# Optimization experiments

Hardware: AMD Instinct MI355X
Metric: run time of the kernel (lower is better)

Reference implementation:

```python
import jax, jax.numpy as jnp
import numpy as np

B, S, F, D, H, L, FF, M, NH, D2, O = 4, 1024, 20, 512, 8, 4, 2048, 32, 3, 256, 1
HD = D // H


def ln(x, g, b, eps=1e-5):
    m = jnp.mean(x, -1, keepdims=True)
    v = jnp.mean((x - m) ** 2, -1, keepdims=True)
    return (x - m) / jnp.sqrt(v + eps) * g + b


def posenc(seq_len, d_model):
    pos = jnp.arange(seq_len, dtype=jnp.float32)[:, None]
    div = jnp.exp(jnp.arange(0, d_model, 2, dtype=jnp.float32) * (-np.log(10000.0) / d_model))
    pe = jnp.zeros((seq_len, d_model), jnp.float32)
    pe = pe.at[:, 0::2].set(jnp.sin(pos * div)).at[:, 1::2].set(jnp.cos(pos * div))
    return pe


def setup_inputs():
    key = jax.random.key(0)
    ks = iter(jax.random.split(key, 64))
    g = lambda shape, s=0.02: jax.random.normal(next(ks), shape, jnp.float32) * s
    z = lambda shape: jnp.zeros(shape, jnp.float32)
    o = lambda shape: jnp.ones(shape, jnp.float32)
    return {
        'x': jax.random.normal(next(ks), (B, S, F), jnp.float32),
        'in_W': g((F, D)), 'in_b': z((D,)), 'in_ln_g': o((D,)), 'in_ln_b': z((D,)),
        'ln1_g': o((L, D)), 'ln1_b': z((L, D)),
        'Wq': g((L, D, D)), 'bq': z((L, D)), 'Wk': g((L, D, D)), 'bk': z((L, D)),
        'Wv': g((L, D, D)), 'bv': z((L, D)), 'Wo': g((L, D, D)), 'bo': z((L, D)),
        'rel': g((L, 2 * M + 1, HD)),
        'ln2_g': o((L, D)), 'ln2_b': z((L, D)),
        'W1': g((L, D, FF)), 'b1': z((L, FF)), 'W2': g((L, FF, D)), 'b2': z((L, D)),
        'gWq': g((D, D)), 'gbq': z((D,)), 'gWk': g((D, D)), 'gbk': z((D,)),
        'gWv': g((D, D)), 'gbv': z((D,)), 'gWo': g((D, D)), 'gbo': z((D,)),
        'hW1': g((NH, D, D2)), 'hb1': z((NH, D2)), 'hln_g': o((NH, D2)), 'hln_b': z((NH, D2)),
        'hW2': g((NH, D2, O)), 'hb2': z((NH, O)),
    }


def _heads(xx, Wq, bq, Wk, bk, Wv, bv):
    # project and split into heads -> [B,H,S,HD]
    q = (xx @ Wq + bq).reshape(B, S, H, HD).transpose(0, 2, 1, 3)
    k = (xx @ Wk + bk).reshape(B, S, H, HD).transpose(0, 2, 1, 3)
    v = (xx @ Wv + bv).reshape(B, S, H, HD).transpose(0, 2, 1, 3)
    return q, k, v


def _block(x, l1g, l1b, Wq, bq, Wk, bk, Wv, bv, Wo, bo, rel, l2g, l2b, W1, b1, W2, b2):
    xn = ln(x, l1g, l1b)
    q, k, v = _heads(xn, Wq, bq, Wk, bk, Wv, bv)
    scores = jnp.einsum('bhqd,bhkd->bhqk', q, k) / jnp.sqrt(jnp.float32(HD))
    pos = jnp.arange(S)
    rel_idx = jnp.clip(pos[None, :] - pos[:, None], -M, M) + M  # [S,S]
    rel_enc = rel[rel_idx]  # [S,S,HD]
    # relative-position bias (NOT scaled by sqrt(HD), matching the torch code)
    scores = scores + jnp.einsum('bhqd,qkd->bhqk', q, rel_enc)
    w = jax.nn.softmax(scores, axis=-1)
    out = jnp.einsum('bhqk,bhkd->bhqd', w, v).transpose(0, 2, 1, 3).reshape(B, S, D)
    x = x + out @ Wo + bo
    xn = ln(x, l2g, l2b)
    ff = jax.nn.gelu(xn @ W1 + b1, approximate=False) @ W2 + b2
    return x + ff


def _forward(x, in_W, in_b, in_ln_g, in_ln_b, ln1_g, ln1_b, Wq, bq, Wk, bk, Wv, bv, Wo, bo, rel,
             ln2_g, ln2_b, W1, b1, W2, b2, gWq, gbq, gWk, gbk, gWv, gbv, gWo, gbo,
             hW1, hb1, hln_g, hln_b, hW2, hb2):
    h = ln(x @ in_W + in_b, in_ln_g, in_ln_b)
    h = h + posenc(S, D)[None]
    for l in range(L):
        h = _block(h, ln1_g[l], ln1_b[l], Wq[l], bq[l], Wk[l], bk[l], Wv[l], bv[l],
                   Wo[l], bo[l], rel[l], ln2_g[l], ln2_b[l], W1[l], b1[l], W2[l], b2[l])
    # global multi-head self-attention (standard scaled dot-product)
    q, k, v = _heads(h, gWq, gbq, gWk, gbk, gWv, gbv)
    w = jax.nn.softmax(jnp.einsum('bhqd,bhkd->bhqk', q, k) / jnp.sqrt(jnp.float32(HD)), axis=-1)
    go = jnp.einsum('bhqk,bhkd->bhqd', w, v).transpose(0, 2, 1, 3).reshape(B, S, D) @ gWo + gbo
    ctx = go[:, -1, :]  # last-timestep context [B,D]
    y = jnp.einsum('bd,hde->bhe', ctx, hW1) + hb1  # [B,NH,D2]
    y = jax.nn.relu(ln(y, hln_g, hln_b))
    return jnp.einsum('bhe,heo->bho', y, hW2) + hb2  # [B,NH,O]


def reference(x, in_W, in_b, in_ln_g, in_ln_b, ln1_g, ln1_b, Wq, bq, Wk, bk, Wv, bv, Wo, bo, rel,
              ln2_g, ln2_b, W1, b1, W2, b2, gWq, gbq, gWk, gbk, gWv, gbv, gWo, gbo,
              hW1, hb1, hln_g, hln_b, hW2, hb2):
    return _forward(x, in_W, in_b, in_ln_g, in_ln_b, ln1_g, ln1_b, Wq, bq, Wk, bk, Wv, bv, Wo, bo,
                    rel, ln2_g, ln2_b, W1, b1, W2, b2, gWq, gbq, gWk, gbk, gWv, gbv, gWo, gbo,
                    hW1, hb1, hln_g, hln_b, hW2, hb2)
```

## Files before the change

kernel.cpp:

```cpp
#include <hip/hip_runtime.h>
#include <math.h>

#define DEV __device__ __forceinline__

constexpr int BSD = 4 * 1024 * 512;

typedef __attribute__((ext_vector_type(8))) short bf16x8;
typedef __attribute__((ext_vector_type(4))) float f32x4;

typedef __attribute__((address_space(1))) const void global_cvoid;
typedef __attribute__((address_space(3))) void lds_void;

DEV ushort f2b(float f) {
  union { float f; uint u; } x{f};
  uint r = x.u + 0x7fff + ((x.u >> 16) & 1);
  return (ushort)(r >> 16);
}
DEV float b2f(ushort u) {
  union { uint u; float f; } x{(uint)u << 16};
  return x.f;
}
DEV int swz128(int b) { return b ^ (((b >> 7) & 7) << 4); }

DEV float wave_sum(float v) {
#pragma unroll
  for (int m = 32; m >= 1; m >>= 1) v += __shfl_xor(v, m, 64);
  return v;
}
DEV float wave_max(float v) {
#pragma unroll
  for (int m = 32; m >= 1; m >>= 1) v = fmaxf(v, __shfl_xor(v, m, 64));
  return v;
}
DEV float block_sum(float v, float* sm) {
  v = wave_sum(v);
  __syncthreads();
  if ((threadIdx.x & 63) == 0) sm[threadIdx.x >> 6] = v;
  __syncthreads();
  return sm[0] + sm[1] + sm[2] + sm[3];
}
DEV float block_max(float v, float* sm) {
  v = wave_max(v);
  __syncthreads();
  if ((threadIdx.x & 63) == 0) sm[threadIdx.x >> 6] = v;
  __syncthreads();
  return fmaxf(fmaxf(sm[0], sm[1]), fmaxf(sm[2], sm[3]));
}

__global__ __launch_bounds__(256) void k_inproj(
    const float* __restrict__ x, const float* __restrict__ W,
    const float* __restrict__ bias, const float* __restrict__ g,
    const float* __restrict__ bt, float* __restrict__ h) {
  int r = blockIdx.x;
  int s = r & 1023;
  int t = threadIdx.x;
  __shared__ float xr[20];
  __shared__ float red[4];
  if (t < 20) xr[t] = x[r * 20 + t];
  __syncthreads();
  float o0 = bias[t], o1 = bias[t + 256];
#pragma unroll
  for (int f = 0; f < 20; f++) {
    float xv = xr[f];
    o0 += xv * W[f * 512 + t];
    o1 += xv * W[f * 512 + t + 256];
  }
  float mean = block_sum(o0 + o1, red) * (1.f / 512.f);
  float d0 = o0 - mean, d1 = o1 - mean;
  float var = block_sum(d0 * d0 + d1 * d1, red) * (1.f / 512.f);
  float rs = rsqrtf(var + 1e-5f);
  float n0 = d0 * rs * g[t] + bt[t];
  float n1 = d1 * rs * g[t + 256] + bt[t + 256];
  const float c1 = -9.210340371976184f / 512.f;
  {
    int c = t;
    float div = expf((float)(c & ~1) * c1);
    float arg = (float)s * div;
    n0 += (c & 1) ? cosf(arg) : sinf(arg);
  }
  {
    int c = t + 256;
    float div = expf((float)(c & ~1) * c1);
    float arg = (float)s * div;
    n1 += (c & 1) ? cosf(arg) : sinf(arg);
  }
  float* hr = h + (size_t)r * 512;
  hr[t] = n0;
  hr[t + 256] = n1;
}

__global__ __launch_bounds__(256) void k_lnb(
    const float* __restrict__ x, const float* __restrict__ g,
    const float* __restrict__ bt, ushort* __restrict__ y) {
  __shared__ float red[4];
  int r = blockIdx.x;
  int t = threadIdx.x;
  const float* xr = x + (size_t)r * 512;
  float v0 = xr[t], v1 = xr[t + 256];
  float mean = block_sum(v0 + v1, red) * (1.f / 512.f);
  float d0 = v0 - mean, d1 = v1 - mean;
  float var = block_sum(d0 * d0 + d1 * d1, red) * (1.f / 512.f);
  float rs = rsqrtf(var + 1e-5f);
  ushort* yr = y + (size_t)r * 512;
  yr[t] = f2b(d0 * rs * g[t] + bt[t]);
  yr[t + 256] = f2b(d1 * rs * g[t + 256] + bt[t + 256]);
}

struct PJobs {
  const float* s[19];
  ushort* d[19];
};
__global__ __launch_bounds__(256) void k_wprep(PJobs j, int K, int N) {
  const float* src = j.s[blockIdx.z];
  ushort* dst = j.d[blockIdx.z];
  __shared__ float ld[32][33];
  int n0 = blockIdx.x * 32, k0 = blockIdx.y * 32;
  int c = threadIdx.x & 31, r0 = threadIdx.x >> 5;
#pragma unroll
  for (int i = 0; i < 4; i++)
    ld[r0 + i * 8][c] = src[(size_t)(k0 + r0 + i * 8) * N + n0 + c];
  __syncthreads();
#pragma unroll
  for (int i = 0; i < 4; i++)
    dst[(size_t)(n0 + r0 + i * 8) * K + k0 + c] = f2b(ld[c][r0 + i * 8]);
}

__global__ __launch_bounds__(256) void k_relprep(const float* __restrict__ rel,
                                                 ushort* __restrict__ relb) {
  int i = blockIdx.x * 256 + threadIdx.x;
  int l = blockIdx.y;
  int r = i >> 6, d = i & 63;
  float v = (r < 65) ? rel[((size_t)l * 65 + r) * 64 + d] * 8.f : 0.f;
  relb[(size_t)l * 80 * 64 + i] = f2b(v);
}

__global__ __launch_bounds__(256) void k_vprep(const ushort* __restrict__ qkv,
                                               ushort* __restrict__ vT) {
  int bh = blockIdx.z, b = bh >> 3, h = bh & 7;
  int s0 = blockIdx.x * 32, d0 = blockIdx.y * 32;
  __shared__ ushort td[32][33];
  int c = threadIdx.x & 31, r = threadIdx.x >> 5;
#pragma unroll
  for (int i = 0; i < 4; i++)
    td[r + i * 8][c] =
        qkv[(size_t)(b * 1024 + s0 + r + i * 8) * 1536 + 1024 + h * 64 + d0 + c];
  __syncthreads();
#pragma unroll
  for (int i = 0; i < 4; i++)
    vT[((size_t)bh * 64 + d0 + r + i * 8) * 1024 + s0 + c] = td[c][r + i * 8];
}

template <int BM, int BN, int MODE, int FUSEB>
__global__ __launch_bounds__(256) void k_mg(
    const ushort* __restrict__ A, const ushort* __restrict__ Bt,
    const float* __restrict__ bias0, const float* __restrict__ bias1,
    const float* __restrict__ bias2, void* __restrict__ Cv,
    ushort* __restrict__ C2, int K, int ldc, int gx) {
  constexpr int BK = 64;
  __shared__ __align__(16) ushort As[BM * BK];
  __shared__ __align__(16) ushort Bs[BN * BK];
  int nwg = gridDim.x;
  int id = blockIdx.x;
  int logical = (id & 7) * (nwg >> 3) + (id >> 3);
  int bx = logical % gx, by = logical / gx;
  int row0 = by * BM, col0 = bx * BN;
  int t = threadIdx.x, lane = t & 63, w = t >> 6;
  int rl15 = lane & 15, l16 = lane >> 4;
  constexpr int WR = (BM == 128 && BN == 128) ? 2 : BM / 32;
  constexpr int WC = 4 / WR;
  constexpr int MI = BM / (WR * 16);
  constexpr int NI = BN / (WC * 16);
  int wr = w % WR, wc = w / WR;
  int wrow = wr * MI * 16;
  int wcol = wc * NI * 16;
  f32x4 acc[MI][NI] = {};
  for (int kb = 0; kb < K; kb += BK) {
    __syncthreads();
#pragma unroll
    for (int i = 0; i < BM / 32; i++) {
      int blk = w * (BM / 32) + i;
      int lb = blk * 1024 + lane * 16;
      int lg = swz128(lb);
      int r = lg >> 7, cb = (lg & 127) >> 1;
      __builtin_amdgcn_global_load_lds(
          (global_cvoid*)(A + (size_t)(row0 + r) * K + kb + cb),
          (lds_void*)((char*)As + blk * 1024), 16, 0, 0);
    }
#pragma unroll
    for (int i = 0; i < BN / 32; i++) {
      int blk = w * (BN / 32) + i;
      int lb = blk * 1024 + lane * 16;
      int lg = swz128(lb);
      int r = lg >> 7, cb = (lg & 127) >> 1;
      __builtin_amdgcn_global_load_lds(
          (global_cvoid*)(Bt + (size_t)(col0 + r) * K + kb + cb),
          (lds_void*)((char*)Bs + blk * 1024), 16, 0, 0);
    }
    __syncthreads();
#pragma unroll
    for (int ks = 0; ks < 2; ks++) {
      bf16x8 af[MI], bfr[NI];
#pragma unroll
      for (int mi = 0; mi < MI; mi++) {
        int row = wrow + mi * 16 + rl15;
        af[mi] = *(const bf16x8*)((char*)As + swz128(row * 128 + ks * 64 + l16 * 16));
      }
#pragma unroll
      for (int ni = 0; ni < NI; ni++) {
        int row = wcol + ni * 16 + rl15;
        bfr[ni] = *(const bf16x8*)((char*)Bs + swz128(row * 128 + ks * 64 + l16 * 16));
      }
#pragma unroll
      for (int mi = 0; mi < MI; mi++)
#pragma unroll
        for (int ni = 0; ni < NI; ni++)
          acc[mi][ni] = __builtin_amdgcn_mfma_f32_16x16x32_bf16(af[mi], bfr[ni],
                                                                acc[mi][ni], 0, 0, 0);
    }
  }
#pragma unroll
  for (int mi = 0; mi < MI; mi++) {
#pragma unroll
    for (int ni = 0; ni < NI; ni++) {
      int col = col0 + wcol + ni * 16 + rl15;
      float bv;
      if (FUSEB) {
        const float* bp = bias0;
        int c = col;
        if (c >= 1024) { bp = bias2; c -= 1024; }
        else if (c >= 512) { bp = bias1; c -= 512; }
        bv = bp[c];
      } else {
        bv = bias0[col];
      }
#pragma unroll
      for (int r = 0; r < 4; r++) {
        int row = row0 + wrow + mi * 16 + l16 * 4 + r;
        float val = acc[mi][ni][r] + bv;
        if (FUSEB && col < 512) val *= 0.125f;
        if (MODE == 0) {
          ((ushort*)Cv)[(size_t)row * ldc + col] = f2b(val);
        } else if (MODE == 1) {
          float* Cp = (float*)Cv + (size_t)row * ldc + col;
          *Cp = *Cp + val;
        } else if (MODE == 2) {
          val = 0.5f * val * (1.f + erff(val * 0.70710678118654752f));
          ((ushort*)Cv)[(size_t)row * ldc + col] = f2b(val);
        } else {
          float* Cp = (float*)Cv + (size_t)row * ldc + col;
          float nv = *Cp + val;
          *Cp = nv;
          C2[(size_t)row * ldc + col] = f2b(nv);
        }
      }
    }
  }
}

__global__ __launch_bounds__(256) void k_attn_mfma(
    const ushort* __restrict__ qkv, const ushort* __restrict__ vT,
    const ushort* __restrict__ relb, ushort* __restrict__ ao) {
  __shared__ __align__(16) ushort Ks[64 * 64];
  __shared__ __align__(16) ushort Vts[64 * 64];
  __shared__ ushort qrlb[64][66];
  __shared__ __align__(16) ushort Pl[4][16 * 72];
  int t = threadIdx.x, lane = t & 63, w = t >> 6;
  int h = blockIdx.y, b = blockIdx.z;
  int q0 = blockIdx.x * 64;
  size_t baseq = ((size_t)b * 1024) * 1536 + h * 64;
  size_t basek = baseq + 512;
  const ushort* vTb = vT + ((size_t)(b * 8 + h)) * 64 * 1024;
  int qw = q0 + w * 16;
  int rl15 = lane & 15, l16 = lane >> 4;

  bf16x8 aq[2];
#pragma unroll
  for (int ks = 0; ks < 2; ks++)
    aq[ks] = *(const bf16x8*)(qkv + baseq + (size_t)(qw + rl15) * 1536 + ks * 32 + l16 * 8);

#pragma unroll
  for (int nb = 0; nb < 5; nb++) {
    f32x4 rc = {};
#pragma unroll
    for (int ks = 0; ks < 2; ks++) {
      bf16x8 rb = *(const bf16x8*)(relb + (size_t)(nb * 16 + rl15) * 64 + ks * 32 + l16 * 8);
      rc = __builtin_amdgcn_mfma_f32_16x16x32_bf16(aq[ks], rb, rc, 0, 0, 0);
    }
    int col = nb * 16 + rl15;
    if (col < 65) {
#pragma unroll
      for (int r = 0; r < 4; r++) qrlb[w * 16 + l16 * 4 + r][col] = f2b(rc[r]);
    }
  }

  float mrow[4], lrow[4];
  f32x4 oacc[4] = {};
#pragma unroll
  for (int r = 0; r < 4; r++) {
    mrow[r] = -1e30f;
    lrow[r] = 0.f;
  }

  for (int kb = 0; kb < 1024; kb += 64) {
    __syncthreads();
#pragma unroll
    for (int i = 0; i < 2; i++) {
      int blk = w * 2 + i;
      int lb = blk * 1024 + lane * 16;
      int lg = swz128(lb);
      int r = lg >> 7, cb = (lg & 127) >> 1;
      __builtin_amdgcn_global_load_lds(
          (global_cvoid*)(qkv + basek + (size_t)(kb + r) * 1536 + cb),
          (lds_void*)((char*)Ks + blk * 1024), 16, 0, 0);
      __builtin_amdgcn_global_load_lds(
          (global_cvoid*)(vTb + (size_t)r * 1024 + kb + cb),
          (lds_void*)((char*)Vts + blk * 1024), 16, 0, 0);
    }
    __syncthreads();

    f32x4 sacc[4] = {};
#pragma unroll
    for (int ks = 0; ks < 2; ks++) {
#pragma unroll
      for (int nb = 0; nb < 4; nb++) {
        bf16x8 bk8 = *(const bf16x8*)((char*)Ks +
                                      swz128((nb * 16 + rl15) * 128 + ks * 64 + l16 * 16));
        sacc[nb] = __builtin_amdgcn_mfma_f32_16x16x32_bf16(aq[ks], bk8, sacc[nb], 0, 0, 0);
      }
    }

    float sv[4][4];
    bool hiU = (kb >= qw + 47);
    bool loU = (kb + 95 <= qw);
    if (hiU || loU) {
      int idx = hiU ? 64 : 0;
#pragma unroll
      for (int r = 0; r < 4; r++) {
        float crow = b2f(qrlb[w * 16 + l16 * 4 + r][idx]);
#pragma unroll
        for (int nb = 0; nb < 4; nb++) sv[r][nb] = sacc[nb][r] + crow;
      }
    } else {
#pragma unroll
      for (int r = 0; r < 4; r++) {
        int rloc = l16 * 4 + r;
        int qg = q0 + w * 16 + rloc;
#pragma unroll
        for (int nb = 0; nb < 4; nb++) {
          int delta = kb + nb * 16 + rl15 - qg;
          delta = delta < -32 ? -32 : (delta > 32 ? 32 : delta);
          sv[r][nb] = sacc[nb][r] + b2f(qrlb[w * 16 + rloc][delta + 32]);
        }
      }
    }

    float p[4][4];
#pragma unroll
    for (int r = 0; r < 4; r++) {
      float rowm = fmaxf(fmaxf(sv[r][0], sv[r][1]), fmaxf(sv[r][2], sv[r][3]));
#pragma unroll
      for (int msk = 1; msk <= 8; msk <<= 1)
        rowm = fmaxf(rowm, __shfl_xor(rowm, msk, 64));
      if (rowm > mrow[r]) {
        float scale = __expf(mrow[r] - rowm);
        mrow[r] = rowm;
        lrow[r] *= scale;
#pragma unroll
        for (int nb = 0; nb < 4; nb++) oacc[nb][r] *= scale;
      }
      float ls = 0.f;
#pragma unroll
      for (int nb = 0; nb < 4; nb++) {
        float pv = __expf(sv[r][nb] - mrow[r]);
        p[nb][r] = pv;
        ls += pv;
      }
#pragma unroll
      for (int msk = 1; msk <= 8; msk <<= 1) ls += __shfl_xor(ls, msk, 64);
      lrow[r] += ls;
    }

#pragma unroll
    for (int nb = 0; nb < 4; nb++)
#pragma unroll
      for (int r = 0; r < 4; r++)
        Pl[w][(l16 * 4 + r) * 72 + nb * 16 + rl15] = f2b(p[nb][r]);
#pragma unroll
    for (int ks = 0; ks < 2; ks++) {
      bf16x8 pa = *(const bf16x8*)&Pl[w][rl15 * 72 + ks * 32 + l16 * 8];
#pragma unroll
      for (int nb = 0; nb < 4; nb++) {
        bf16x8 bv8 = *(const bf16x8*)((char*)Vts +
                                      swz128((nb * 16 + rl15) * 128 + ks * 64 + l16 * 16));
        oacc[nb] = __builtin_amdgcn_mfma_f32_16x16x32_bf16(pa, bv8, oacc[nb], 0, 0, 0);
      }
    }
  }

  size_t baseo = ((size_t)b * 1024) * 512 + h * 64;
#pragma unroll
  for (int nb = 0; nb < 4; nb++) {
    int d = nb * 16 + rl15;
#pragma unroll
    for (int r = 0; r < 4; r++) {
      int row = q0 + w * 16 + l16 * 4 + r;
      ao[baseo + (size_t)row * 512 + d] = f2b(oacc[nb][r] / lrow[r]);
    }
  }
}

__global__ __launch_bounds__(256) void k_gattn(
    const ushort* __restrict__ qkv, float* __restrict__ ctxa) {
  int t = threadIdx.x;
  int h = blockIdx.x & 7, b = blockIdx.x >> 3;
  __shared__ float Qs[64];
  __shared__ float sc[1024];
  __shared__ float red[4];
  __shared__ float op[4][64];
  if (t < 64) Qs[t] = b2f(qkv[(size_t)(b * 1024 + 1023) * 1536 + h * 64 + t]);
  __syncthreads();
  float lm = -1e30f;
  float sv[4];
#pragma unroll
  for (int jj = 0; jj < 4; jj++) {
    int j = t + (jj << 8);
    float s = 0.f;
#pragma unroll
    for (int d = 0; d < 64; d++)
      s += Qs[d] * b2f(qkv[(size_t)(b * 1024 + j) * 1536 + 512 + h * 64 + d]);
    sv[jj] = s;
    lm = fmaxf(lm, s);
  }
  float bm = block_max(lm, red);
  float ls = 0.f;
#pragma unroll
  for (int jj = 0; jj < 4; jj++) {
    float e = __expf(sv[jj] - bm);
    sc[t + (jj << 8)] = e;
    ls += e;
  }
  float bs = block_sum(ls, red);
  int d = t & 63, qd = t >> 6;
  float acc = 0.f;
  for (int j = qd << 8; j < (qd << 8) + 256; j++)
    acc += sc[j] * b2f(qkv[(size_t)(b * 1024 + j) * 1536 + 1024 + h * 64 + d]);
  op[qd][d] = acc;
  __syncthreads();
  if (t < 64) {
    float r = (op[0][t] + op[1][t] + op[2][t] + op[3][t]) / bs;
    ctxa[b * 512 + h * 64 + t] = r;
  }
}

__global__ __launch_bounds__(256) void k_rowgemm(
    const float* __restrict__ xrow, const float* __restrict__ W,
    const float* __restrict__ bias, float* __restrict__ y) {
  int b = blockIdx.x;
  int t = threadIdx.x;
  __shared__ float xs[512];
  xs[t] = xrow[b * 512 + t];
  xs[t + 256] = xrow[b * 512 + t + 256];
  __syncthreads();
  float a0 = bias[t], a1 = bias[t + 256];
  for (int kk = 0; kk < 512; kk++) {
    float xv = xs[kk];
    a0 += xv * W[(size_t)kk * 512 + t];
    a1 += xv * W[(size_t)kk * 512 + t + 256];
  }
  y[b * 512 + t] = a0;
  y[b * 512 + t + 256] = a1;
}

__global__ __launch_bounds__(256) void k_head(
    const float* __restrict__ ctx, const float* __restrict__ hW1,
    const float* __restrict__ hb1, const float* __restrict__ hg,
    const float* __restrict__ hbt, const float* __restrict__ hW2,
    const float* __restrict__ hb2, float* __restrict__ out) {
  int b = blockIdx.x / 3, nh = blockIdx.x % 3;
  int t = threadIdx.x;
  __shared__ float cs[512];
  __shared__ float red[4];
  cs[t] = ctx[b * 512 + t];
  cs[t + 256] = ctx[b * 512 + t + 256];
  __syncthreads();
  float y = hb1[nh * 256 + t];
  for (int d = 0; d < 512; d++) y += cs[d] * hW1[((size_t)nh * 512 + d) * 256 + t];
  float mean = block_sum(y, red) * (1.f / 256.f);
  float dv = y - mean;
  float var = block_sum(dv * dv, red) * (1.f / 256.f);
  float rs = rsqrtf(var + 1e-5f);
  float yn = dv * rs * hg[nh * 256 + t] + hbt[nh * 256 + t];
  yn = fmaxf(yn, 0.f);
  float s = block_sum(yn * hW2[nh * 256 + t], red);
  if (t == 0) out[b * 3 + nh] = s + hb2[nh];
}

extern "C" void kernel_launch(void* const* d_in, const int* in_sizes, int n_in,
                              void* d_out, int out_size, void* d_ws, size_t ws_size,
                              hipStream_t stream) {
  const float* x = (const float*)d_in[0];
  const float* in_W = (const float*)d_in[1];
  const float* in_b = (const float*)d_in[2];
  const float* in_lng = (const float*)d_in[3];
  const float* in_lnb = (const float*)d_in[4];
  const float* ln1_g = (const float*)d_in[5];
  const float* ln1_b = (const float*)d_in[6];
  const float* Wq = (const float*)d_in[7];
  const float* bq = (const float*)d_in[8];
  const float* Wk = (const float*)d_in[9];
  const float* bk = (const float*)d_in[10];
  const float* Wv = (const float*)d_in[11];
  const float* bv = (const float*)d_in[12];
  const float* Wo = (const float*)d_in[13];
  const float* bo = (const float*)d_in[14];
  const float* rel = (const float*)d_in[15];
  const float* ln2_g = (const float*)d_in[16];
  const float* ln2_b = (const float*)d_in[17];
  const float* W1 = (const float*)d_in[18];
  const float* b1 = (const float*)d_in[19];
  const float* W2 = (const float*)d_in[20];
  const float* b2 = (const float*)d_in[21];
  const float* gWq = (const float*)d_in[22];
  const float* gbq = (const float*)d_in[23];
  const float* gWk = (const float*)d_in[24];
  const float* gbk = (const float*)d_in[25];
  const float* gWv = (const float*)d_in[26];
  const float* gbv = (const float*)d_in[27];
  const float* gWo = (const float*)d_in[28];
  const float* gbo = (const float*)d_in[29];
  const float* hW1 = (const float*)d_in[30];
  const float* hb1 = (const float*)d_in[31];
  const float* hlng = (const float*)d_in[32];
  const float* hlnb = (const float*)d_in[33];
  const float* hW2 = (const float*)d_in[34];
  const float* hb2 = (const float*)d_in[35];
  float* out = (float*)d_out;

  uint8_t* wsb = (uint8_t*)d_ws;
  const size_t MB = 1024 * 1024;
  float* h = (float*)(wsb + 0);
  ushort* xn = (ushort*)(wsb + 8 * MB);
  ushort* qkvb = (ushort*)(wsb + 12 * MB);
  ushort* aob = (ushort*)(wsb + 24 * MB);
  ushort* ffb = (ushort*)(wsb + 28 * MB);
  ushort* vTb = ffb;
  ushort* wqkv = (ushort*)(wsb + 44 * MB);
  ushort* wto = (ushort*)(wsb + 50 * MB);
  ushort* wt1 = (ushort*)(wsb + 52 * MB);
  ushort* wt2 = (ushort*)(wsb + 60 * MB);
  ushort* gwqkv = (ushort*)(wsb + 68 * MB);
  ushort* relb = (ushort*)(wsb + 70 * MB);
  float* attnlast = (float*)(wsb + 71 * MB);
  float* ctx = attnlast + 4096;

  const size_t W55 = 512 * 512;

  {
    PJobs j{};
    for (int l = 0; l < 4; l++) {
      j.s[l * 4 + 0] = Wq + (size_t)l * W55;
      j.d[l * 4 + 0] = wqkv + (size_t)l * 1536 * 512;
      j.s[l * 4 + 1] = Wk + (size_t)l * W55;
      j.d[l * 4 + 1] = wqkv + (size_t)l * 1536 * 512 + 512 * 512;
      j.s[l * 4 + 2] = Wv + (size_t)l * W55;
      j.d[l * 4 + 2] = wqkv + (size_t)l * 1536 * 512 + 1024 * 512;
      j.s[l * 4 + 3] = Wo + (size_t)l * W55;
      j.d[l * 4 + 3] = wto + (size_t)l * W55;
    }
    j.s[16] = gWq; j.d[16] = gwqkv;
    j.s[17] = gWk; j.d[17] = gwqkv + 512 * 512;
    j.s[18] = gWv; j.d[18] = gwqkv + 1024 * 512;
    k_wprep<<<dim3(16, 16, 19), 256, 0, stream>>>(j, 512, 512);
  }
  {
    PJobs j{};
    for (int l = 0; l < 4; l++) {
      j.s[l] = W1 + (size_t)l * 512 * 2048;
      j.d[l] = wt1 + (size_t)l * 2048 * 512;
    }
    k_wprep<<<dim3(64, 16, 4), 256, 0, stream>>>(j, 512, 2048);
  }
  {
    PJobs j{};
    for (int l = 0; l < 4; l++) {
      j.s[l] = W2 + (size_t)l * 2048 * 512;
      j.d[l] = wt2 + (size_t)l * 512 * 2048;
    }
    k_wprep<<<dim3(16, 64, 4), 256, 0, stream>>>(j, 2048, 512);
  }
  k_relprep<<<dim3(20, 4), 256, 0, stream>>>(rel, relb);
  k_inproj<<<4096, 256, 0, stream>>>(x, in_W, in_b, in_lng, in_lnb, h);

  for (int l = 0; l < 4; l++) {
    size_t vo = (size_t)l * 512;
    k_lnb<<<4096, 256, 0, stream>>>(h, ln1_g + vo, ln1_b + vo, xn);
    k_mg<128, 64, 0, 1><<<768, 256, 0, stream>>>(xn, wqkv + (size_t)l * 1536 * 512,
                                                 bq + vo, bk + vo, bv + vo, qkvb,
                                                 nullptr, 512, 1536, 24);
    k_vprep<<<dim3(32, 2, 32), 256, 0, stream>>>(qkvb, vTb);
    k_attn_mfma<<<dim3(16, 8, 4), 256, 0, stream>>>(qkvb, vTb,
                                                    relb + (size_t)l * 80 * 64, aob);
    k_mg<64, 64, 1, 0><<<512, 256, 0, stream>>>(aob, wto + (size_t)l * W55, bo + vo,
                                                nullptr, nullptr, h, nullptr, 512, 512, 8);
    k_lnb<<<4096, 256, 0, stream>>>(h, ln2_g + vo, ln2_b + vo, xn);
    k_mg<128, 128, 2, 0><<<512, 256, 0, stream>>>(xn, wt1 + (size_t)l * 2048 * 512,
                                                  b1 + (size_t)l * 2048, nullptr, nullptr,
                                                  ffb, nullptr, 512, 2048, 16);
    if (l < 3)
      k_mg<64, 64, 1, 0><<<512, 256, 0, stream>>>(ffb, wt2 + (size_t)l * 512 * 2048,
                                                  b2 + vo, nullptr, nullptr, h, nullptr,
                                                  2048, 512, 8);
    else
      k_mg<64, 64, 3, 0><<<512, 256, 0, stream>>>(ffb, wt2 + (size_t)l * 512 * 2048,
                                                  b2 + vo, nullptr, nullptr, h, xn,
                                                  2048, 512, 8);
  }

  k_mg<128, 64, 0, 1><<<768, 256, 0, stream>>>(xn, gwqkv, gbq, gbk, gbv, qkvb,
                                               nullptr, 512, 1536, 24);
  k_gattn<<<32, 256, 0, stream>>>(qkvb, attnlast);
  k_rowgemm<<<4, 256, 0, stream>>>(attnlast, gWo, gbo, ctx);
  k_head<<<12, 256, 0, stream>>>(ctx, hW1, hb1, hlng, hlnb, hW2, hb2, out);
}
```

Before: 621.9 us.

## Split attention keys across waves, fuse V transpose into QKV GEMM, wave-level layernorm

The layernorm now gives each 64-lane wave one row and uses float4 loads and wave reductions, so it runs as 1024 blocks instead of 4096 block-reduced ones. The separate V-transpose kernel is removed, and the QKV GEMM epilogue writes V transposed directly. Attention now uses 512 threads, with two wave groups each covering half the keys and merging softmax state through LDS. K and V tiles are read straight from global memory instead of being staged in LDS with async loads, which cuts launches and increases parallelism but risks higher global traffic and scattered transposed writes in the epilogue.

```diff
diff --git a/kernel.cpp b/kernel.cpp
--- a/kernel.cpp
+++ b/kernel.cpp
@@ -89,21 +89,33 @@
   hr[t + 256] = n1;
 }
 
-__global__ __launch_bounds__(256) void k_lnb(
+__global__ __launch_bounds__(256) void k_lnw(
     const float* __restrict__ x, const float* __restrict__ g,
     const float* __restrict__ bt, ushort* __restrict__ y) {
-  __shared__ float red[4];
-  int r = blockIdx.x;
-  int t = threadIdx.x;
-  const float* xr = x + (size_t)r * 512;
-  float v0 = xr[t], v1 = xr[t + 256];
-  float mean = block_sum(v0 + v1, red) * (1.f / 512.f);
-  float d0 = v0 - mean, d1 = v1 - mean;
-  float var = block_sum(d0 * d0 + d1 * d1, red) * (1.f / 512.f);
+  int lane = threadIdx.x & 63;
+  int r = blockIdx.x * 4 + (threadIdx.x >> 6);
+  const float4* xr = (const float4*)(x + (size_t)r * 512);
+  float4 a = xr[lane];
+  float4 c = xr[lane + 64];
+  float s = a.x + a.y + a.z + a.w + c.x + c.y + c.z + c.w;
+  float mean = wave_sum(s) * (1.f / 512.f);
+  float d0 = a.x - mean, d1 = a.y - mean, d2 = a.z - mean, d3 = a.w - mean;
+  float e0 = c.x - mean, e1 = c.y - mean, e2 = c.z - mean, e3 = c.w - mean;
+  float vs = d0 * d0 + d1 * d1 + d2 * d2 + d3 * d3 +
+             e0 * e0 + e1 * e1 + e2 * e2 + e3 * e3;
+  float var = wave_sum(vs) * (1.f / 512.f);
   float rs = rsqrtf(var + 1e-5f);
-  ushort* yr = y + (size_t)r * 512;
-  yr[t] = f2b(d0 * rs * g[t] + bt[t]);
-  yr[t + 256] = f2b(d1 * rs * g[t + 256] + bt[t + 256]);
+  const float4* g4 = (const float4*)g;
+  const float4* b4 = (const float4*)bt;
+  float4 g0 = g4[lane], g1 = g4[lane + 64];
+  float4 b0 = b4[lane], b1 = b4[lane + 64];
+  ushort4 o0 = {f2b(d0 * rs * g0.x + b0.x), f2b(d1 * rs * g0.y + b0.y),
+                f2b(d2 * rs * g0.z + b0.z), f2b(d3 * rs * g0.w + b0.w)};
+  ushort4 o1 = {f2b(e0 * rs * g1.x + b1.x), f2b(e1 * rs * g1.y + b1.y),
+                f2b(e2 * rs * g1.z + b1.z), f2b(e3 * rs * g1.w + b1.w)};
+  ushort4* yr = (ushort4*)(y + (size_t)r * 512);
+  yr[lane] = o0;
+  yr[lane + 64] = o1;
 }
 
 struct PJobs {
@@ -132,22 +144,6 @@
   int r = i >> 6, d = i & 63;
   float v = (r < 65) ? rel[((size_t)l * 65 + r) * 64 + d] * 8.f : 0.f;
   relb[(size_t)l * 80 * 64 + i] = f2b(v);
-}
-
-__global__ __launch_bounds__(256) void k_vprep(const ushort* __restrict__ qkv,
-                                               ushort* __restrict__ vT) {
-  int bh = blockIdx.z, b = bh >> 3, h = bh & 7;
-  int s0 = blockIdx.x * 32, d0 = blockIdx.y * 32;
-  __shared__ ushort td[32][33];
-  int c = threadIdx.x & 31, r = threadIdx.x >> 5;
-#pragma unroll
-  for (int i = 0; i < 4; i++)
-    td[r + i * 8][c] =
-        qkv[(size_t)(b * 1024 + s0 + r + i * 8) * 1536 + 1024 + h * 64 + d0 + c];
-  __syncthreads();
-#pragma unroll
-  for (int i = 0; i < 4; i++)
-    vT[((size_t)bh * 64 + d0 + r + i * 8) * 1024 + s0 + c] = td[c][r + i * 8];
 }
 
 template <int BM, int BN, int MODE, int FUSEB>
@@ -239,7 +235,13 @@
         float val = acc[mi][ni][r] + bv;
         if (FUSEB && col < 512) val *= 0.125f;
         if (MODE == 0) {
-          ((ushort*)Cv)[(size_t)row * ldc + col] = f2b(val);
+          ushort bval = f2b(val);
+          ((ushort*)Cv)[(size_t)row * ldc + col] = bval;
+          if (FUSEB && col >= 1024) {
+            int dg = col - 1024;
+            int bh = (row >> 10) * 8 + (dg >> 6);
+            C2[((size_t)bh * 64 + (dg & 63)) * 1024 + (row & 1023)] = bval;
+          }
         } else if (MODE == 1) {
           float* Cp = (float*)Cv + (size_t)row * ldc + col;
           *Cp = *Cp + val;
@@ -257,41 +259,46 @@
   }
 }
 
-__global__ __launch_bounds__(256) void k_attn_mfma(
+__global__ __launch_bounds__(512, 4) void k_attn2(
     const ushort* __restrict__ qkv, const ushort* __restrict__ vT,
     const ushort* __restrict__ relb, ushort* __restrict__ ao) {
-  __shared__ __align__(16) ushort Ks[64 * 64];
-  __shared__ __align__(16) ushort Vts[64 * 64];
-  __shared__ ushort qrlb[64][66];
-  __shared__ __align__(16) ushort Pl[4][16 * 72];
+  __shared__ ushort qrlb[4][16][66];
+  __shared__ __align__(16) ushort Pl[8][16 * 72];
+  __shared__ float Om[4][16][64];
+  __shared__ float Ml[4][16][2];
   int t = threadIdx.x, lane = t & 63, w = t >> 6;
+  int wq = w & 3, kh = w >> 2;
   int h = blockIdx.y, b = blockIdx.z;
   int q0 = blockIdx.x * 64;
+  int qw = q0 + wq * 16;
+  int rl15 = lane & 15, l16 = lane >> 4;
   size_t baseq = ((size_t)b * 1024) * 1536 + h * 64;
   size_t basek = baseq + 512;
   const ushort* vTb = vT + ((size_t)(b * 8 + h)) * 64 * 1024;
-  int qw = q0 + w * 16;
-  int rl15 = lane & 15, l16 = lane >> 4;
 
   bf16x8 aq[2];
 #pragma unroll
   for (int ks = 0; ks < 2; ks++)
     aq[ks] = *(const bf16x8*)(qkv + baseq + (size_t)(qw + rl15) * 1536 + ks * 32 + l16 * 8);
 
-#pragma unroll
-  for (int nb = 0; nb < 5; nb++) {
-    f32x4 rc = {};
-#pragma unroll
-    for (int ks = 0; ks < 2; ks++) {
-      bf16x8 rb = *(const bf16x8*)(relb + (size_t)(nb * 16 + rl15) * 64 + ks * 32 + l16 * 8);
-      rc = __builtin_amdgcn_mfma_f32_16x16x32_bf16(aq[ks], rb, rc, 0, 0, 0);
-    }
-    int col = nb * 16 + rl15;
-    if (col < 65) {
-#pragma unroll
-      for (int r = 0; r < 4; r++) qrlb[w * 16 + l16 * 4 + r][col] = f2b(rc[r]);
-    }
-  }
+  if (w < 4) {
+#pragma unroll
+    for (int nb = 0; nb < 5; nb++) {
+      f32x4 rc = {};
+#pragma unroll
+      for (int ks = 0; ks < 2; ks++) {
+        bf16x8 rb =
+            *(const bf16x8*)(relb + (size_t)(nb * 16 + rl15) * 64 + ks * 32 + l16 * 8);
+        rc = __builtin_amdgcn_mfma_f32_16x16x32_bf16(aq[ks], rb, rc, 0, 0, 0);
+      }
+      int col = nb * 16 + rl15;
+      if (col < 65) {
+#pragma unroll
+        for (int r = 0; r < 4; r++) qrlb[wq][l16 * 4 + r][col] = f2b(rc[r]);
+      }
+    }
+  }
+  __syncthreads();
 
   float mrow[4], lrow[4];
   f32x4 oacc[4] = {};
@@ -301,30 +308,16 @@
     lrow[r] = 0.f;
   }
 
-  for (int kb = 0; kb < 1024; kb += 64) {
-    __syncthreads();
-#pragma unroll
-    for (int i = 0; i < 2; i++) {
-      int blk = w * 2 + i;
-      int lb = blk * 1024 + lane * 16;
-      int lg = swz128(lb);
-      int r = lg >> 7, cb = (lg & 127) >> 1;
-      __builtin_amdgcn_global_load_lds(
-          (global_cvoid*)(qkv + basek + (size_t)(kb + r) * 1536 + cb),
-          (lds_void*)((char*)Ks + blk * 1024), 16, 0, 0);
-      __builtin_amdgcn_global_load_lds(
-          (global_cvoid*)(vTb + (size_t)r * 1024 + kb + cb),
-          (lds_void*)((char*)Vts + blk * 1024), 16, 0, 0);
-    }
-    __syncthreads();
-
+  for (int kt = 0; kt < 8; kt++) {
+    int kb = (kh << 9) + (kt << 6);
     f32x4 sacc[4] = {};
 #pragma unroll
     for (int ks = 0; ks < 2; ks++) {
 #pragma unroll
       for (int nb = 0; nb < 4; nb++) {
-        bf16x8 bk8 = *(const bf16x8*)((char*)Ks +
-                                      swz128((nb * 16 + rl15) * 128 + ks * 64 + l16 * 16));
+        bf16x8 bk8 = *(const bf16x8*)(qkv + basek +
+                                      (size_t)(kb + nb * 16 + rl15) * 1536 +
+                                      ks * 32 + l16 * 8);
         sacc[nb] = __builtin_amdgcn_mfma_f32_16x16x32_bf16(aq[ks], bk8, sacc[nb], 0, 0, 0);
       }
     }
@@ -336,7 +329,7 @@
       int idx = hiU ? 64 : 0;
 #pragma unroll
       for (int r = 0; r < 4; r++) {
-        float crow = b2f(qrlb[w * 16 + l16 * 4 + r][idx]);
+        float crow = b2f(qrlb[wq][l16 * 4 + r][idx]);
 #pragma unroll
         for (int nb = 0; nb < 4; nb++) sv[r][nb] = sacc[nb][r] + crow;
       }
@@ -344,12 +337,12 @@
 #pragma unroll
       for (int r = 0; r < 4; r++) {
         int rloc = l16 * 4 + r;
-        int qg = q0 + w * 16 + rloc;
+        int qg = q0 + wq * 16 + rloc;
 #pragma unroll
         for (int nb = 0; nb < 4; nb++) {
           int delta = kb + nb * 16 + rl15 - qg;
           delta = delta < -32 ? -32 : (delta > 32 ? 32 : delta);
-          sv[r][nb] = sacc[nb][r] + b2f(qrlb[w * 16 + rloc][delta + 32]);
+          sv[r][nb] = sacc[nb][r] + b2f(qrlb[wq][rloc][delta + 32]);
         }
       }
     }
@@ -390,21 +383,41 @@
       bf16x8 pa = *(const bf16x8*)&Pl[w][rl15 * 72 + ks * 32 + l16 * 8];
 #pragma unroll
       for (int nb = 0; nb < 4; nb++) {
-        bf16x8 bv8 = *(const bf16x8*)((char*)Vts +
-                                      swz128((nb * 16 + rl15) * 128 + ks * 64 + l16 * 16));
+        bf16x8 bv8 = *(const bf16x8*)(vTb + (size_t)(nb * 16 + rl15) * 1024 + kb +
+                                      ks * 32 + l16 * 8);
         oacc[nb] = __builtin_amdgcn_mfma_f32_16x16x32_bf16(pa, bv8, oacc[nb], 0, 0, 0);
       }
     }
   }
 
-  size_t baseo = ((size_t)b * 1024) * 512 + h * 64;
-#pragma unroll
-  for (int nb = 0; nb < 4; nb++) {
-    int d = nb * 16 + rl15;
+  if (w >= 4) {
+#pragma unroll
+    for (int nb = 0; nb < 4; nb++)
+#pragma unroll
+      for (int r = 0; r < 4; r++) Om[wq][l16 * 4 + r][nb * 16 + rl15] = oacc[nb][r];
+    if (rl15 == 0) {
+#pragma unroll
+      for (int r = 0; r < 4; r++) {
+        Ml[wq][l16 * 4 + r][0] = mrow[r];
+        Ml[wq][l16 * 4 + r][1] = lrow[r];
+      }
+    }
+  }
+  __syncthreads();
+  if (w < 4) {
+    size_t baseo = ((size_t)b * 1024) * 512 + h * 64;
 #pragma unroll
     for (int r = 0; r < 4; r++) {
-      int row = q0 + w * 16 + l16 * 4 + r;
-      ao[baseo + (size_t)row * 512 + d] = f2b(oacc[nb][r] / lrow[r]);
+      int row = l16 * 4 + r;
+      float m2 = Ml[wq][row][0], l2 = Ml[wq][row][1];
+      float mn = fmaxf(mrow[r], m2);
+      float s1 = __expf(mrow[r] - mn), s2 = __expf(m2 - mn);
+      float linv = 1.f / (lrow[r] * s1 + l2 * s2);
+#pragma unroll
+      for (int nb = 0; nb < 4; nb++) {
+        float val = (oacc[nb][r] * s1 + Om[wq][row][nb * 16 + rl15] * s2) * linv;
+        ao[baseo + (size_t)(qw + row) * 512 + nb * 16 + rl15] = f2b(val);
+      }
     }
   }
 }
@@ -593,16 +606,15 @@
 
   for (int l = 0; l < 4; l++) {
     size_t vo = (size_t)l * 512;
-    k_lnb<<<4096, 256, 0, stream>>>(h, ln1_g + vo, ln1_b + vo, xn);
+    k_lnw<<<1024, 256, 0, stream>>>(h, ln1_g + vo, ln1_b + vo, xn);
     k_mg<128, 64, 0, 1><<<768, 256, 0, stream>>>(xn, wqkv + (size_t)l * 1536 * 512,
                                                  bq + vo, bk + vo, bv + vo, qkvb,
-                                                 nullptr, 512, 1536, 24);
-    k_vprep<<<dim3(32, 2, 32), 256, 0, stream>>>(qkvb, vTb);
-    k_attn_mfma<<<dim3(16, 8, 4), 256, 0, stream>>>(qkvb, vTb,
-                                                    relb + (size_t)l * 80 * 64, aob);
+                                                 vTb, 512, 1536, 24);
+    k_attn2<<<dim3(16, 8, 4), 512, 0, stream>>>(qkvb, vTb,
+                                                relb + (size_t)l * 80 * 64, aob);
     k_mg<64, 64, 1, 0><<<512, 256, 0, stream>>>(aob, wto + (size_t)l * W55, bo + vo,
                                                 nullptr, nullptr, h, nullptr, 512, 512, 8);
-    k_lnb<<<4096, 256, 0, stream>>>(h, ln2_g + vo, ln2_b + vo, xn);
+    k_lnw<<<1024, 256, 0, stream>>>(h, ln2_g + vo, ln2_b + vo, xn);
     k_mg<128, 128, 2, 0><<<512, 256, 0, stream>>>(xn, wt1 + (size_t)l * 2048 * 512,
                                                   b1 + (size_t)l * 2048, nullptr, nullptr,
                                                   ffb, nullptr, 512, 2048, 16);
@@ -617,7 +629,7 @@
   }
 
   k_mg<128, 64, 0, 1><<<768, 256, 0, stream>>>(xn, gwqkv, gbq, gbk, gbv, qkvb,
-                                               nullptr, 512, 1536, 24);
+                                               vTb, 512, 1536, 24);
   k_gattn<<<32, 256, 0, stream>>>(qkvb, attnlast);
   k_rowgemm<<<4, 256, 0, stream>>>(attnlast, gWo, gbo, ctx);
   k_head<<<12, 256, 0, stream>>>(ctx, hW1, hb1, hlng, hlnb, hW2, hb2, out);
```

New measurement: 695.8 us. 11.9% more time.
